# Kernel tuning notes

Hardware: AMD Instinct MI355X
Metric: run time of the kernel (lower is better)

Reference implementation:

```python
import jax, jax.numpy as jnp
import numpy as np

ANNEAL_T_START = 5.0
T_END = 1.0


def setup_inputs() -> dict:
    key = jax.random.key(0)
    ks = jax.random.split(key, 8)
    B, V, H, CD, WID = 8192, 1024, 128, 16, 64
    return {
        "cond": jax.random.normal(ks[0], (B, CD), jnp.float32),
        "W": 0.01 * jax.random.normal(ks[1], (V, H), jnp.float32),
        "b": 0.01 * jax.random.normal(ks[2], (V,), jnp.float32),
        "c": 0.01 * jax.random.normal(ks[3], (H,), jnp.float32),
        "fc1_w": jax.random.normal(ks[4], (WID, CD), jnp.float32) / np.float32(np.sqrt(CD)),
        "fc1_b": jnp.zeros((WID,), jnp.float32),
        "fc2_w": jax.random.normal(ks[5], (2 * (V + H), WID), jnp.float32) / np.float32(np.sqrt(WID)),
        "fc2_b": jnp.zeros((2 * (V + H),), jnp.float32),
        "falloff": jnp.float32(1.0),
        "steps": 16,
    }


def _bern(key, p):
    # Bernoulli sample as float of same dtype as p.
    return (jax.random.uniform(key, p.shape, p.dtype) < p).astype(p.dtype)


def reference(cond, W, b, c, fc1_w, fc1_b, fc2_w, fc2_b, falloff, steps):
    V, H = W.shape
    B = cond.shape[0]
    dtype = W.dtype

    # Conditioner: FiLM-style modulation of visible/hidden biases.
    x = jnp.tanh(cond @ fc1_w.T + fc1_b)
    x = x @ fc2_w.T + fc2_b  # [B, 2*(V+H)]
    gamma_b = x[:, :V]
    beta_b = x[:, V:2 * V]
    gamma_c = x[:, 2 * V:2 * V + H]
    beta_c = x[:, 2 * V + H:]
    b_mod = (1.0 + gamma_b) * b + beta_b  # [B, V]
    c_mod = (1.0 + gamma_c) * c + beta_c  # [B, H]
    bsum = jnp.sum(b_mod, axis=-1)  # [B], constant across steps

    # Annealing temperature schedule (sigmoid falloff).
    t = jnp.arange(steps, dtype=dtype)
    s = 1.0 / (1.0 + jnp.exp(falloff * (t - steps / 2.0)))
    temps = T_END + (ANNEAL_T_START - T_END) * s  # [steps]

    base = jax.random.key(42)
    v0 = _bern(jax.random.fold_in(base, 2 ** 20), jnp.full((B, V), 0.5, dtype))
    s0_0 = jnp.ones((B, 1), dtype)

    def flip(v, s0):
        return s0 * v + (1.0 - s0) * (1.0 - v)

    def step(carry, xs):
        v, s0 = carry
        i, T = xs
        k1, k2, k3 = jax.random.split(jax.random.fold_in(base, i), 3)
        v_eff = flip(v, s0)
        p_h = jax.nn.sigmoid((v_eff @ W + c_mod) / T)  # [B, H]
        h = _bern(k1, p_h)
        a = h @ W.T  # [B, V]
        vb = jnp.sum(v * b_mod, axis=-1)
        va = jnp.sum(v * a, axis=-1)
        dE = -bsum - jnp.sum(a, axis=-1) + 2.0 * vb + 2.0 * va  # [B]
        p_s0 = jax.nn.sigmoid(dE / T)
        s0n = _bern(k2, p_s0)[:, None]  # [B, 1]
        p_v = jax.nn.sigmoid((a + b_mod) / T)
        v_samp = _bern(k3, p_v)
        v_next = flip(v_samp, s0n)
        return (v_next, s0n), None

    (v, _), _ = jax.lax.scan(
        step, (v0, s0_0), (jnp.arange(steps, dtype=jnp.int32), temps)
    )
    return v
```

## Files before the change

### kernel.cpp

```cpp
#include <hip/hip_runtime.h>
#include <stdint.h>

#pragma clang fp contract(off)

#define B_ 8192
#define V_ 1024
#define H_ 128
#define CD_ 16
#define WID_ 64
#define NOUT_ 2304
#define STEPS_ 16

__host__ __device__ __forceinline__ void tf2x32(uint32_t k0, uint32_t k1,
                                                uint32_t x0, uint32_t x1,
                                                uint32_t* o0, uint32_t* o1) {
  uint32_t ks2 = k0 ^ k1 ^ 0x1BD11BDAu;
#define RL_(v, d) (((v) << (d)) | ((v) >> (32 - (d))))
#define RND_(a) { x0 += x1; x1 = RL_(x1, a); x1 ^= x0; }
  x0 += k0; x1 += k1;
  RND_(13) RND_(15) RND_(26) RND_(6)
  x0 += k1; x1 += ks2 + 1u;
  RND_(17) RND_(29) RND_(16) RND_(24)
  x0 += ks2; x1 += k0 + 2u;
  RND_(13) RND_(15) RND_(26) RND_(6)
  x0 += k0; x1 += k1 + 3u;
  RND_(17) RND_(29) RND_(16) RND_(24)
  x0 += k1; x1 += ks2 + 4u;
  RND_(13) RND_(15) RND_(26) RND_(6)
  x0 += ks2; x1 += k0 + 5u;
#undef RND_
#undef RL_
  *o0 = x0; *o1 = x1;
}

struct Keys { uint32_t a[6]; };

__device__ __forceinline__ uint32_t draw_bits(uint32_t ka, uint32_t kb, uint32_t j) {
  uint32_t x0, x1;
  tf2x32(ka, kb, 0u, j, &x0, &x1);
  return x0 ^ x1;
}

__device__ __forceinline__ float bits_to_u(uint32_t bits) {
  return __fsub_rn(__uint_as_float((bits >> 9) | 0x3f800000u), 1.0f);
}

__device__ __forceinline__ float exp_a(float x) {
  float xc = fminf(fmaxf(x, -88.3762626647949f), 88.3762626647950f);
  float fx = floorf(__fadd_rn(__fmul_rn(xc, 1.44269504088896341f), 0.5f));
  float xr = __fsub_rn(xc, __fmul_rn(0.693359375f, fx));
  xr = __fsub_rn(xr, __fmul_rn(-2.12194440e-4f, fx));
  float zz = __fmul_rn(xr, xr);
  float y = 1.9875691500E-4f;
  y = __fadd_rn(__fmul_rn(y, xr), 1.3981999507E-3f);
  y = __fadd_rn(__fmul_rn(y, xr), 8.3334519073E-3f);
  y = __fadd_rn(__fmul_rn(y, xr), 4.1665795894E-2f);
  y = __fadd_rn(__fmul_rn(y, xr), 1.6666665459E-1f);
  y = __fadd_rn(__fmul_rn(y, xr), 5.0000001201E-1f);
  y = __fadd_rn(__fmul_rn(y, zz), xr);
  y = __fadd_rn(y, 1.0f);
  int n = (int)fx;
  float sc = __int_as_float((n + 127) << 23);
  return __fmul_rn(y, sc);
}

__device__ __forceinline__ float tanh_a(float xin) {
  float x = fmaxf(fminf(xin, 7.90531110763549805f), -7.90531110763549805f);
  float x2 = __fmul_rn(x, x);
  float p = __fadd_rn(__fmul_rn(x2, -2.76076847742355e-16f), 2.00018790482477e-13f);
  p = __fadd_rn(__fmul_rn(x2, p), -8.60467152213735e-11f);
  p = __fadd_rn(__fmul_rn(x2, p), 5.12229709037114e-08f);
  p = __fadd_rn(__fmul_rn(x2, p), 1.48572235717979e-05f);
  p = __fadd_rn(__fmul_rn(x2, p), 6.37261928875436e-04f);
  p = __fadd_rn(__fmul_rn(x2, p), 4.89352455891786e-03f);
  p = __fmul_rn(x, p);
  float q = __fadd_rn(__fmul_rn(x2, 1.19825839466702e-06f), 1.18534705686654e-04f);
  q = __fadd_rn(__fmul_rn(x2, q), 2.26843463243900e-03f);
  q = __fadd_rn(__fmul_rn(x2, q), 4.89352518554385e-03f);
  float r = p / q;
  if (fabsf(xin) < 0.0004f) r = xin;
  return r;
}

__device__ __forceinline__ float sigmoid_a(float z) {
  float e = exp_a(-z);
  return 1.0f / __fadd_rn(1.0f, e);
}

__device__ __forceinline__ float maskf(float wv, uint32_t sm) {
  return __uint_as_float(__float_as_uint(wv) & sm);
}

__global__ void k_transpose(const float* __restrict__ W, float* __restrict__ WT,
                            const float* __restrict__ fc2w, float* __restrict__ fc2T) {
  int i = blockIdx.x * blockDim.x + threadIdx.x;
  if (i < V_ * H_) { int v = i / H_, h = i % H_; WT[h * V_ + v] = W[i]; }
  if (i < NOUT_ * WID_) { int j = i / WID_, w = i % WID_; fc2T[w * NOUT_ + j] = fc2w[i]; }
}

__global__ void k_temps(const float* __restrict__ falloff, float* __restrict__ temps) {
  int t = threadIdx.x;
  if (t < 16) {
    float arg = __fmul_rn(*falloff, __fsub_rn((float)t, 8.0f));
    float e = exp_a(arg);
    float s = 1.0f / __fadd_rn(1.0f, e);
    temps[t] = __fadd_rn(1.0f, __fmul_rn(4.0f, s));
  }
}

__global__ void k_mlp1(const float* __restrict__ cond, const float* __restrict__ fc1w,
                       const float* __restrict__ fc1b, float* __restrict__ xout) {
  int idx = blockIdx.x * blockDim.x + threadIdx.x;
  if (idx >= B_ * WID_) return;
  int row = idx >> 6, w = idx & 63;
  float acc = 0.0f;
  for (int k = 0; k < CD_; k++) acc = __fmaf_rn(cond[row * CD_ + k], fc1w[w * CD_ + k], acc);
  float z = __fadd_rn(acc, fc1b[w]);
  xout[idx] = tanh_a(z);
}

__global__ __launch_bounds__(128) void k_mlp2b(const float* __restrict__ xmlp,
                       const float* __restrict__ fc2T, const float* __restrict__ fc2b,
                       const float* __restrict__ bvec, float* __restrict__ b_mod) {
  __shared__ float xs[32][WID_];
  int jbase = blockIdx.x * 128;
  int r0 = blockIdx.y * 32;
  int tid = threadIdx.x;
  for (int t = tid; t < 32 * WID_; t += 128)
    xs[t >> 6][t & 63] = xmlp[(r0 + (t >> 6)) * WID_ + (t & 63)];
  __syncthreads();
  int j = jbase + tid;
  float accg[32], accb[32];
#pragma unroll
  for (int r = 0; r < 32; r++) { accg[r] = 0.0f; accb[r] = 0.0f; }
  for (int w = 0; w < WID_; w++) {
    float fg = fc2T[w * NOUT_ + j];
    float fb = fc2T[w * NOUT_ + 1024 + j];
#pragma unroll
    for (int r = 0; r < 32; r++) {
      float xv = xs[r][w];
      accg[r] = __fmaf_rn(xv, fg, accg[r]);
      accb[r] = __fmaf_rn(xv, fb, accb[r]);
    }
  }
  float bj = bvec[j];
  float biasg = fc2b[j], biasb = fc2b[1024 + j];
#pragma unroll
  for (int r = 0; r < 32; r++) {
    float g = __fadd_rn(accg[r], biasg);
    float bb = __fadd_rn(accb[r], biasb);
    float t1 = __fadd_rn(1.0f, g);
    b_mod[(r0 + r) * V_ + j] = __fadd_rn(__fmul_rn(t1, bj), bb);
  }
}

__global__ __launch_bounds__(128) void k_mlp2c(const float* __restrict__ xmlp,
                       const float* __restrict__ fc2T, const float* __restrict__ fc2b,
                       const float* __restrict__ cvec, float* __restrict__ c_mod) {
  __shared__ float xs[32][WID_];
  int r0 = blockIdx.y * 32;
  int tid = threadIdx.x;
  for (int t = tid; t < 32 * WID_; t += 128)
    xs[t >> 6][t & 63] = xmlp[(r0 + (t >> 6)) * WID_ + (t & 63)];
  __syncthreads();
  float accg[32], accb[32];
#pragma unroll
  for (int r = 0; r < 32; r++) { accg[r] = 0.0f; accb[r] = 0.0f; }
  for (int w = 0; w < WID_; w++) {
    float fg = fc2T[w * NOUT_ + 2048 + tid];
    float fb = fc2T[w * NOUT_ + 2176 + tid];
#pragma unroll
    for (int r = 0; r < 32; r++) {
      float xv = xs[r][w];
      accg[r] = __fmaf_rn(xv, fg, accg[r]);
      accb[r] = __fmaf_rn(xv, fb, accb[r]);
    }
  }
  float cj = cvec[tid];
  float biasg = fc2b[2048 + tid], biasb = fc2b[2176 + tid];
#pragma unroll
  for (int r = 0; r < 32; r++) {
    float g = __fadd_rn(accg[r], biasg);
    float bb = __fadd_rn(accb[r], biasb);
    float t1 = __fadd_rn(1.0f, g);
    c_mod[(r0 + r) * H_ + tid] = __fadd_rn(__fmul_rn(t1, cj), bb);
  }
}

__global__ __launch_bounds__(64) void k_bsum(const float* __restrict__ b_mod,
                                             float* __restrict__ bsum) {
  int row = blockIdx.x * 64 + threadIdx.x;
  const float4* bp = (const float4*)(b_mod + (size_t)row * V_);
  float acc = 0.0f;
  for (int c = 0; c < 32; c++) {
    float4 Bv[8];
#pragma unroll
    for (int q = 0; q < 8; q++) Bv[q] = bp[c * 8 + q];
#pragma unroll
    for (int q = 0; q < 8; q++) {
      acc = __fadd_rn(acc, Bv[q].x);
      acc = __fadd_rn(acc, Bv[q].y);
      acc = __fadd_rn(acc, Bv[q].z);
      acc = __fadd_rn(acc, Bv[q].w);
    }
  }
  bsum[row] = acc;
}

__global__ void k_v0(float* __restrict__ vout, uint32_t* __restrict__ v_bits,
                     float* __restrict__ s0, uint32_t kva, uint32_t kvb) {
  int idx = blockIdx.x * blockDim.x + threadIdx.x;
  int row = idx >> 10, col = idx & 1023;
  uint32_t bits = draw_bits(kva, kvb, (uint32_t)idx);
  float u = bits_to_u(bits);
  float v = (u < 0.5f) ? 1.0f : 0.0f;
  vout[idx] = v;
  unsigned long long m = __ballot(v == 1.0f);
  if ((threadIdx.x & 63) == 0) {
    v_bits[row * 32 + (col >> 5)] = (uint32_t)m;
    v_bits[row * 32 + (col >> 5) + 1] = (uint32_t)(m >> 32);
  }
  if (col == 0) s0[row] = 1.0f;
}

__global__ __launch_bounds__(256) void k_h(const float* __restrict__ W,
                   const float* __restrict__ c_mod, const uint32_t* __restrict__ v_bits,
                   const float* __restrict__ s0, uint32_t* __restrict__ h_bits,
                   const float* __restrict__ temps, int step, Keys kn) {
  __shared__ uint32_t nib[16][32];
  int tid = threadIdx.x;
  int ct = tid & 31;
  int rt = tid >> 5;
  int h0 = ct << 2;
  int row0 = blockIdx.x * 16 + rt * 2;
  float T = temps[step];
  float acc0[4] = {0.f, 0.f, 0.f, 0.f};
  float acc1[4] = {0.f, 0.f, 0.f, 0.f};
  uint32_t flip0 = (s0[row0] == 0.0f) ? 0xFFFFFFFFu : 0u;
  uint32_t flip1 = (s0[row0 + 1] == 0.0f) ? 0xFFFFFFFFu : 0u;
  const uint4* vb0 = (const uint4*)(v_bits + (size_t)row0 * 32);
  const uint4* vb1 = (const uint4*)(v_bits + (size_t)(row0 + 1) * 32);
  const float* wbase = W + h0;

  auto sect = [&](uint32_t w0, uint32_t w1, const float* wp) {
    uint32_t m0 = __brev(w0) ^ flip0;
    uint32_t m1 = __brev(w1) ^ flip1;
    for (int j4 = 0; j4 < 8; j4++) {
#pragma unroll
      for (int jj = 0; jj < 4; jj++) {
        float4 wv = *(const float4*)(wp + (size_t)jj * H_);
        uint32_t s0m = (uint32_t)((int32_t)m0 >> 31);
        uint32_t s1m = (uint32_t)((int32_t)m1 >> 31);
        m0 <<= 1; m1 <<= 1;
        acc0[0] = __fadd_rn(acc0[0], maskf(wv.x, s0m));
        acc0[1] = __fadd_rn(acc0[1], maskf(wv.y, s0m));
        acc0[2] = __fadd_rn(acc0[2], maskf(wv.z, s0m));
        acc0[3] = __fadd_rn(acc0[3], maskf(wv.w, s0m));
        acc1[0] = __fadd_rn(acc1[0], maskf(wv.x, s1m));
        acc1[1] = __fadd_rn(acc1[1], maskf(wv.y, s1m));
        acc1[2] = __fadd_rn(acc1[2], maskf(wv.z, s1m));
        acc1[3] = __fadd_rn(acc1[3], maskf(wv.w, s1m));
      }
      wp += (size_t)4 * H_;
    }
  };

  for (int kq = 0; kq < 8; kq++) {
    uint4 q0 = vb0[kq];
    uint4 q1 = vb1[kq];
    const float* wk = wbase + (size_t)(kq * 128) * H_;
    sect(q0.x, q1.x, wk);
    sect(q0.y, q1.y, wk + (size_t)32 * H_);
    sect(q0.z, q1.z, wk + (size_t)64 * H_);
    sect(q0.w, q1.w, wk + (size_t)96 * H_);
  }

  uint32_t nib0 = 0, nib1 = 0;
  float4 cm0 = *(const float4*)(c_mod + (size_t)row0 * H_ + h0);
  float4 cm1 = *(const float4*)(c_mod + (size_t)(row0 + 1) * H_ + h0);
  const float cm0a[4] = {cm0.x, cm0.y, cm0.z, cm0.w};
  const float cm1a[4] = {cm1.x, cm1.y, cm1.z, cm1.w};
#pragma unroll
  for (int e = 0; e < 4; e++) {
    float z0 = __fadd_rn(acc0[e], cm0a[e]) / T;
    float p0 = sigmoid_a(z0);
    uint32_t b0 = draw_bits(kn.a[0], kn.a[1], (uint32_t)(row0 * H_ + h0 + e));
    if (bits_to_u(b0) < p0) nib0 |= 1u << e;
    float z1 = __fadd_rn(acc1[e], cm1a[e]) / T;
    float p1 = sigmoid_a(z1);
    uint32_t b1 = draw_bits(kn.a[0], kn.a[1], (uint32_t)((row0 + 1) * H_ + h0 + e));
    if (bits_to_u(b1) < p1) nib1 |= 1u << e;
  }
  nib[rt * 2][ct] = nib0;
  nib[rt * 2 + 1][ct] = nib1;
  __syncthreads();
  if (tid < 64) {
    int rloc = tid >> 2, wq = tid & 3;
    uint32_t word = 0;
#pragma unroll
    for (int i = 0; i < 8; i++) word |= nib[rloc][wq * 8 + i] << (4 * i);
    h_bits[(size_t)(blockIdx.x * 16 + rloc) * 4 + wq] = word;
  }
}

__global__ __launch_bounds__(256) void k_a(const float* __restrict__ WT,
                   const uint32_t* __restrict__ h_bits, float* __restrict__ a) {
  int tid = threadIdx.x;
  int ct = tid & 63;
  int rt = __builtin_amdgcn_readfirstlane(tid >> 6);
  int v0 = blockIdx.x * 256 + (ct << 2);
  int r0 = blockIdx.y * 32 + rt * 8;
  float acc[8][4];
#pragma unroll
  for (int r = 0; r < 8; r++)
#pragma unroll
    for (int e = 0; e < 4; e++) acc[r][e] = 0.0f;
  uint4 hw[8];
#pragma unroll
  for (int r = 0; r < 8; r++) hw[r] = *(const uint4*)(h_bits + (size_t)(r0 + r) * 4);
  const float* wp0 = WT + v0;

  auto asect = [&](int WW, const uint32_t mwin[8]) {
    uint32_t m[8];
#pragma unroll
    for (int r = 0; r < 8; r++) m[r] = __brev(mwin[r]);
    const float* wp = wp0 + (size_t)(WW * 32) * V_;
    for (int j4 = 0; j4 < 8; j4++) {
#pragma unroll
      for (int jj = 0; jj < 4; jj++) {
        float4 wv = *(const float4*)(wp + (size_t)jj * V_);
#pragma unroll
        for (int r = 0; r < 8; r++) {
          uint32_t sm = (uint32_t)((int32_t)m[r] >> 31);
          m[r] <<= 1;
          acc[r][0] = __fadd_rn(acc[r][0], maskf(wv.x, sm));
          acc[r][1] = __fadd_rn(acc[r][1], maskf(wv.y, sm));
          acc[r][2] = __fadd_rn(acc[r][2], maskf(wv.z, sm));
          acc[r][3] = __fadd_rn(acc[r][3], maskf(wv.w, sm));
        }
      }
      wp += (size_t)4 * V_;
    }
  };

  {
    uint32_t mw[8];
#pragma unroll
    for (int r = 0; r < 8; r++) mw[r] = hw[r].x;
    asect(0, mw);
#pragma unroll
    for (int r = 0; r < 8; r++) mw[r] = hw[r].y;
    asect(1, mw);
#pragma unroll
    for (int r = 0; r < 8; r++) mw[r] = hw[r].z;
    asect(2, mw);
#pragma unroll
    for (int r = 0; r < 8; r++) mw[r] = hw[r].w;
    asect(3, mw);
  }

#pragma unroll
  for (int r = 0; r < 8; r++) {
    float4 o = make_float4(acc[r][0], acc[r][1], acc[r][2], acc[r][3]);
    *(float4*)(a + (size_t)(r0 + r) * V_ + v0) = o;
  }
}

__global__ __launch_bounds__(64) void k_s0(const float* __restrict__ a,
                     const float* __restrict__ b_mod, const float* __restrict__ bsum,
                     const uint32_t* __restrict__ v_bits, float* __restrict__ s0,
                     const float* __restrict__ temps, int step, Keys kn) {
  int row = blockIdx.x * 64 + threadIdx.x;
  const float4* ap = (const float4*)(a + (size_t)row * V_);
  const float4* bp = (const float4*)(b_mod + (size_t)row * V_);
  const uint32_t* vbp = v_bits + row * 32;
  float suma = 0.0f, vb = 0.0f, va = 0.0f;
  float4 A0[8], B0[8], A1[8], B1[8];
  uint32_t m0, m1;

  auto LOADC = [&](int c, float4* A, float4* B, uint32_t& m) {
#pragma unroll
    for (int q = 0; q < 8; q++) { A[q] = ap[c * 8 + q]; B[q] = bp[c * 8 + q]; }
    m = vbp[c];
  };
  auto PROC = [&](const float4* A, const float4* B, uint32_t m) {
#pragma unroll
    for (int q = 0; q < 8; q++) {
      const float ax[4] = {A[q].x, A[q].y, A[q].z, A[q].w};
      const float bx[4] = {B[q].x, B[q].y, B[q].z, B[q].w};
#pragma unroll
      for (int e = 0; e < 4; e++) {
        float bit = (float)((m >> (q * 4 + e)) & 1u);
        suma = __fadd_rn(suma, ax[e]);
        vb = __fmaf_rn(bx[e], bit, vb);
        va = __fmaf_rn(ax[e], bit, va);
      }
    }
  };

  LOADC(0, A0, B0, m0);
  for (int cc = 0; cc < 16; cc++) {
    LOADC(2 * cc + 1, A1, B1, m1);
    PROC(A0, B0, m0);
    if (cc < 15) LOADC(2 * cc + 2, A0, B0, m0);
    PROC(A1, B1, m1);
  }

  float dE = __fsub_rn(-bsum[row], suma);
  dE = __fadd_rn(dE, __fmul_rn(2.0f, vb));
  dE = __fadd_rn(dE, __fmul_rn(2.0f, va));
  float T = temps[step];
  float p = sigmoid_a(dE / T);
  uint32_t bits = draw_bits(kn.a[2], kn.a[3], (uint32_t)row);
  float u = bits_to_u(bits);
  s0[row] = (u < p) ? 1.0f : 0.0f;
}

__global__ void k_v(const float* __restrict__ a, const float* __restrict__ b_mod,
                    const float* __restrict__ s0, float* __restrict__ vout,
                    uint32_t* __restrict__ v_bits, const float* __restrict__ temps, int step,
                    Keys kn) {
  int idx = blockIdx.x * blockDim.x + threadIdx.x;
  int row = idx >> 10, col = idx & 1023;
  float T = temps[step];
  float z = __fadd_rn(a[idx], b_mod[idx]) / T;
  float p = sigmoid_a(z);
  uint32_t bits = draw_bits(kn.a[4], kn.a[5], (uint32_t)idx);
  float u = bits_to_u(bits);
  float vs = (u < p) ? 1.0f : 0.0f;
  float vn = (s0[row] != 0.0f) ? vs : (1.0f - vs);
  vout[idx] = vn;
  unsigned long long m = __ballot(vn == 1.0f);
  if ((threadIdx.x & 63) == 0) {
    v_bits[row * 32 + (col >> 5)] = (uint32_t)m;
    v_bits[row * 32 + (col >> 5) + 1] = (uint32_t)(m >> 32);
  }
}

extern "C" void kernel_launch(void* const* d_in, const int* in_sizes, int n_in,
                              void* d_out, int out_size, void* d_ws, size_t ws_size,
                              hipStream_t stream) {
  const float* cond = (const float*)d_in[0];
  const float* W = (const float*)d_in[1];
  const float* bvec = (const float*)d_in[2];
  const float* cvec = (const float*)d_in[3];
  const float* fc1w = (const float*)d_in[4];
  const float* fc1b = (const float*)d_in[5];
  const float* fc2w = (const float*)d_in[6];
  const float* fc2b = (const float*)d_in[7];
  const float* falloff = (const float*)d_in[8];
  float* out = (float*)d_out;

  char* ws = (char*)d_ws;
  size_t off = 0;
  auto alloc = [&](size_t bytes) { void* p = ws + off; off += (bytes + 255) & ~(size_t)255; return p; };
  float* b_mod = (float*)alloc((size_t)B_ * V_ * 4);
  float* c_mod = (float*)alloc((size_t)B_ * H_ * 4);
  float* abuf  = (float*)alloc((size_t)B_ * V_ * 4);
  float* xmlp  = (float*)alloc((size_t)B_ * WID_ * 4);
  float* bsum  = (float*)alloc((size_t)B_ * 4);
  float* s0    = (float*)alloc((size_t)B_ * 4);
  uint32_t* v_bits = (uint32_t*)alloc((size_t)B_ * 32 * 4);
  uint32_t* h_bits = (uint32_t*)alloc((size_t)B_ * 4 * 4);
  float* WT    = (float*)alloc((size_t)H_ * V_ * 4);
  float* fc2T  = (float*)alloc((size_t)WID_ * NOUT_ * 4);
  float* temps = (float*)alloc(16 * 4);

  uint32_t kva, kvb;
  tf2x32(0u, 42u, 0u, 1048576u, &kva, &kvb);
  Keys kn[16];
  for (int i = 0; i < 16; i++) {
    uint32_t f0, f1;
    tf2x32(0u, 42u, 0u, (uint32_t)i, &f0, &f1);
    uint32_t a0, a1;
    tf2x32(f0, f1, 0u, 0u, &a0, &a1); kn[i].a[0] = a0; kn[i].a[1] = a1;
    tf2x32(f0, f1, 0u, 1u, &a0, &a1); kn[i].a[2] = a0; kn[i].a[3] = a1;
    tf2x32(f0, f1, 0u, 2u, &a0, &a1); kn[i].a[4] = a0; kn[i].a[5] = a1;
  }

  k_transpose<<<(NOUT_ * WID_ + 255) / 256, 256, 0, stream>>>(W, WT, fc2w, fc2T);
  k_temps<<<1, 64, 0, stream>>>(falloff, temps);
  k_mlp1<<<(B_ * WID_) / 256, 256, 0, stream>>>(cond, fc1w, fc1b, xmlp);
  k_mlp2b<<<dim3(8, 256), 128, 0, stream>>>(xmlp, fc2T, fc2b, bvec, b_mod);
  k_mlp2c<<<dim3(1, 256), 128, 0, stream>>>(xmlp, fc2T, fc2b, cvec, c_mod);
  k_bsum<<<B_ / 64, 64, 0, stream>>>(b_mod, bsum);
  k_v0<<<(B_ * V_) / 256, 256, 0, stream>>>(out, v_bits, s0, kva, kvb);

  for (int i = 0; i < STEPS_; i++) {
    k_h<<<B_ / 16, 256, 0, stream>>>(W, c_mod, v_bits, s0, h_bits, temps, i, kn[i]);
    k_a<<<dim3(4, B_ / 32), 256, 0, stream>>>(WT, h_bits, abuf);
    k_s0<<<B_ / 64, 64, 0, stream>>>(abuf, b_mod, bsum, v_bits, s0, temps, i, kn[i]);
    k_v<<<(B_ * V_) / 256, 256, 0, stream>>>(abuf, b_mod, s0, out, v_bits, temps, i, kn[i]);
  }
}
```

Baseline: 3.498 ms.

## Use packed FP32 FMA with 0/1 multipliers and give k_h four rows per thread

The masked-add accumulation in k_h and k_a now multiplies each weight by a 0.0 or 1.0 factor taken from the bit mask and uses v_pk_fma_f32, which handles two lanes per instruction. The aim is to halve the VALU instruction count of the inner loops. k_h also moves to 128-thread blocks with four rows per thread, so each weight load is reused across more rows. Adding w*0 instead of a masked zero keeps results the same for finite weights, though the register use of the wider per-thread tile could lower occupancy.

```diff
diff --git a/kernel.cpp b/kernel.cpp
--- a/kernel.cpp
+++ b/kernel.cpp
@@ -10,6 +10,12 @@
 #define WID_ 64
 #define NOUT_ 2304
 #define STEPS_ 16
+
+typedef float f32x2 __attribute__((ext_vector_type(2)));
+
+__device__ __forceinline__ void pkfma(f32x2& acc, f32x2 wv, f32x2 bf2) {
+  asm("v_pk_fma_f32 %0, %1, %2, %0" : "+v"(acc) : "v"(wv), "v"(bf2));
+}
 
 __host__ __device__ __forceinline__ void tf2x32(uint32_t k0, uint32_t k1,
                                                 uint32_t x0, uint32_t x1,
@@ -87,10 +93,6 @@
   return 1.0f / __fadd_rn(1.0f, e);
 }
 
-__device__ __forceinline__ float maskf(float wv, uint32_t sm) {
-  return __uint_as_float(__float_as_uint(wv) & sm);
-}
-
 __global__ void k_transpose(const float* __restrict__ W, float* __restrict__ WT,
                             const float* __restrict__ fc2w, float* __restrict__ fc2T) {
   int i = blockIdx.x * blockDim.x + threadIdx.x;
@@ -223,7 +225,7 @@
   if (col == 0) s0[row] = 1.0f;
 }
 
-__global__ __launch_bounds__(256) void k_h(const float* __restrict__ W,
+__global__ __launch_bounds__(128) void k_h(const float* __restrict__ W,
                    const float* __restrict__ c_mod, const uint32_t* __restrict__ v_bits,
                    const float* __restrict__ s0, uint32_t* __restrict__ h_bits,
                    const float* __restrict__ temps, int step, Keys kn) {
@@ -232,67 +234,74 @@
   int ct = tid & 31;
   int rt = tid >> 5;
   int h0 = ct << 2;
-  int row0 = blockIdx.x * 16 + rt * 2;
+  int row0 = blockIdx.x * 16 + rt * 4;
   float T = temps[step];
-  float acc0[4] = {0.f, 0.f, 0.f, 0.f};
-  float acc1[4] = {0.f, 0.f, 0.f, 0.f};
-  uint32_t flip0 = (s0[row0] == 0.0f) ? 0xFFFFFFFFu : 0u;
-  uint32_t flip1 = (s0[row0 + 1] == 0.0f) ? 0xFFFFFFFFu : 0u;
+  f32x2 acc[4][2];
+#pragma unroll
+  for (int r = 0; r < 4; r++) { acc[r][0] = f32x2{0.f, 0.f}; acc[r][1] = f32x2{0.f, 0.f}; }
+  uint32_t flip[4];
+#pragma unroll
+  for (int r = 0; r < 4; r++) flip[r] = (s0[row0 + r] == 0.0f) ? 0xFFFFFFFFu : 0u;
+  const float* wbase = W + h0;
+
+  auto sect = [&](uint32_t w0, uint32_t w1, uint32_t w2, uint32_t w3, const float* wp) {
+    uint32_t m[4];
+    m[0] = __brev(w0) ^ flip[0];
+    m[1] = __brev(w1) ^ flip[1];
+    m[2] = __brev(w2) ^ flip[2];
+    m[3] = __brev(w3) ^ flip[3];
+    for (int j4 = 0; j4 < 8; j4++) {
+#pragma unroll
+      for (int jj = 0; jj < 4; jj++) {
+        float4 wv = *(const float4*)(wp + (size_t)jj * H_);
+        f32x2 wlo = {wv.x, wv.y};
+        f32x2 whi = {wv.z, wv.w};
+#pragma unroll
+        for (int r = 0; r < 4; r++) {
+          uint32_t sm = (uint32_t)((int32_t)m[r] >> 31);
+          m[r] <<= 1;
+          float bf = __uint_as_float(sm & 0x3f800000u);
+          f32x2 b2 = {bf, bf};
+          pkfma(acc[r][0], wlo, b2);
+          pkfma(acc[r][1], whi, b2);
+        }
+      }
+      wp += (size_t)4 * H_;
+    }
+  };
+
   const uint4* vb0 = (const uint4*)(v_bits + (size_t)row0 * 32);
   const uint4* vb1 = (const uint4*)(v_bits + (size_t)(row0 + 1) * 32);
-  const float* wbase = W + h0;
-
-  auto sect = [&](uint32_t w0, uint32_t w1, const float* wp) {
-    uint32_t m0 = __brev(w0) ^ flip0;
-    uint32_t m1 = __brev(w1) ^ flip1;
-    for (int j4 = 0; j4 < 8; j4++) {
-#pragma unroll
-      for (int jj = 0; jj < 4; jj++) {
-        float4 wv = *(const float4*)(wp + (size_t)jj * H_);
-        uint32_t s0m = (uint32_t)((int32_t)m0 >> 31);
-        uint32_t s1m = (uint32_t)((int32_t)m1 >> 31);
-        m0 <<= 1; m1 <<= 1;
-        acc0[0] = __fadd_rn(acc0[0], maskf(wv.x, s0m));
-        acc0[1] = __fadd_rn(acc0[1], maskf(wv.y, s0m));
-        acc0[2] = __fadd_rn(acc0[2], maskf(wv.z, s0m));
-        acc0[3] = __fadd_rn(acc0[3], maskf(wv.w, s0m));
-        acc1[0] = __fadd_rn(acc1[0], maskf(wv.x, s1m));
-        acc1[1] = __fadd_rn(acc1[1], maskf(wv.y, s1m));
-        acc1[2] = __fadd_rn(acc1[2], maskf(wv.z, s1m));
-        acc1[3] = __fadd_rn(acc1[3], maskf(wv.w, s1m));
-      }
-      wp += (size_t)4 * H_;
-    }
-  };
-
+  const uint4* vb2 = (const uint4*)(v_bits + (size_t)(row0 + 2) * 32);
+  const uint4* vb3 = (const uint4*)(v_bits + (size_t)(row0 + 3) * 32);
   for (int kq = 0; kq < 8; kq++) {
     uint4 q0 = vb0[kq];
     uint4 q1 = vb1[kq];
+    uint4 q2 = vb2[kq];
+    uint4 q3 = vb3[kq];
     const float* wk = wbase + (size_t)(kq * 128) * H_;
-    sect(q0.x, q1.x, wk);
-    sect(q0.y, q1.y, wk + (size_t)32 * H_);
-    sect(q0.z, q1.z, wk + (size_t)64 * H_);
-    sect(q0.w, q1.w, wk + (size_t)96 * H_);
-  }
-
-  uint32_t nib0 = 0, nib1 = 0;
-  float4 cm0 = *(const float4*)(c_mod + (size_t)row0 * H_ + h0);
-  float4 cm1 = *(const float4*)(c_mod + (size_t)(row0 + 1) * H_ + h0);
-  const float cm0a[4] = {cm0.x, cm0.y, cm0.z, cm0.w};
-  const float cm1a[4] = {cm1.x, cm1.y, cm1.z, cm1.w};
-#pragma unroll
-  for (int e = 0; e < 4; e++) {
-    float z0 = __fadd_rn(acc0[e], cm0a[e]) / T;
-    float p0 = sigmoid_a(z0);
-    uint32_t b0 = draw_bits(kn.a[0], kn.a[1], (uint32_t)(row0 * H_ + h0 + e));
-    if (bits_to_u(b0) < p0) nib0 |= 1u << e;
-    float z1 = __fadd_rn(acc1[e], cm1a[e]) / T;
-    float p1 = sigmoid_a(z1);
-    uint32_t b1 = draw_bits(kn.a[0], kn.a[1], (uint32_t)((row0 + 1) * H_ + h0 + e));
-    if (bits_to_u(b1) < p1) nib1 |= 1u << e;
-  }
-  nib[rt * 2][ct] = nib0;
-  nib[rt * 2 + 1][ct] = nib1;
+    sect(q0.x, q1.x, q2.x, q3.x, wk);
+    sect(q0.y, q1.y, q2.y, q3.y, wk + (size_t)32 * H_);
+    sect(q0.z, q1.z, q2.z, q3.z, wk + (size_t)64 * H_);
+    sect(q0.w, q1.w, q2.w, q3.w, wk + (size_t)96 * H_);
+  }
+
+#pragma unroll
+  for (int r = 0; r < 4; r++) {
+    int row = row0 + r;
+    float4 cm = *(const float4*)(c_mod + (size_t)row * H_ + h0);
+    const float cma[4] = {cm.x, cm.y, cm.z, cm.w};
+    const float ac[4] = {acc[r][0][0], acc[r][0][1], acc[r][1][0], acc[r][1][1]};
+    uint32_t nb = 0;
+#pragma unroll
+    for (int e = 0; e < 4; e++) {
+      float z = __fadd_rn(ac[e], cma[e]) / T;
+      float p = sigmoid_a(z);
+      uint32_t b = draw_bits(kn.a[0], kn.a[1], (uint32_t)(row * H_ + h0 + e));
+      if (bits_to_u(b) < p) nb |= 1u << e;
+    }
+    nib[rt * 4 + r][ct] = nb;
+  }
   __syncthreads();
   if (tid < 64) {
     int rloc = tid >> 2, wq = tid & 3;
@@ -307,14 +316,12 @@
                    const uint32_t* __restrict__ h_bits, float* __restrict__ a) {
   int tid = threadIdx.x;
   int ct = tid & 63;
-  int rt = __builtin_amdgcn_readfirstlane(tid >> 6);
+  int rt = tid >> 6;
   int v0 = blockIdx.x * 256 + (ct << 2);
   int r0 = blockIdx.y * 32 + rt * 8;
-  float acc[8][4];
-#pragma unroll
-  for (int r = 0; r < 8; r++)
-#pragma unroll
-    for (int e = 0; e < 4; e++) acc[r][e] = 0.0f;
+  f32x2 acc[8][2];
+#pragma unroll
+  for (int r = 0; r < 8; r++) { acc[r][0] = f32x2{0.f, 0.f}; acc[r][1] = f32x2{0.f, 0.f}; }
   uint4 hw[8];
 #pragma unroll
   for (int r = 0; r < 8; r++) hw[r] = *(const uint4*)(h_bits + (size_t)(r0 + r) * 4);
@@ -329,14 +336,16 @@
 #pragma unroll
       for (int jj = 0; jj < 4; jj++) {
         float4 wv = *(const float4*)(wp + (size_t)jj * V_);
+        f32x2 wlo = {wv.x, wv.y};
+        f32x2 whi = {wv.z, wv.w};
 #pragma unroll
         for (int r = 0; r < 8; r++) {
           uint32_t sm = (uint32_t)((int32_t)m[r] >> 31);
           m[r] <<= 1;
-          acc[r][0] = __fadd_rn(acc[r][0], maskf(wv.x, sm));
-          acc[r][1] = __fadd_rn(acc[r][1], maskf(wv.y, sm));
-          acc[r][2] = __fadd_rn(acc[r][2], maskf(wv.z, sm));
-          acc[r][3] = __fadd_rn(acc[r][3], maskf(wv.w, sm));
+          float bf = __uint_as_float(sm & 0x3f800000u);
+          f32x2 b2 = {bf, bf};
+          pkfma(acc[r][0], wlo, b2);
+          pkfma(acc[r][1], whi, b2);
         }
       }
       wp += (size_t)4 * V_;
@@ -361,7 +370,7 @@
 
 #pragma unroll
   for (int r = 0; r < 8; r++) {
-    float4 o = make_float4(acc[r][0], acc[r][1], acc[r][2], acc[r][3]);
+    float4 o = make_float4(acc[r][0][0], acc[r][0][1], acc[r][1][0], acc[r][1][1]);
     *(float4*)(a + (size_t)(r0 + r) * V_ + v0) = o;
   }
 }
@@ -487,7 +496,7 @@
   k_v0<<<(B_ * V_) / 256, 256, 0, stream>>>(out, v_bits, s0, kva, kvb);
 
   for (int i = 0; i < STEPS_; i++) {
-    k_h<<<B_ / 16, 256, 0, stream>>>(W, c_mod, v_bits, s0, h_bits, temps, i, kn[i]);
+    k_h<<<B_ / 16, 128, 0, stream>>>(W, c_mod, v_bits, s0, h_bits, temps, i, kn[i]);
     k_a<<<dim3(4, B_ / 32), 256, 0, stream>>>(WT, h_bits, abuf);
     k_s0<<<B_ / 64, 64, 0, stream>>>(abuf, b_mod, bsum, v_bits, s0, temps, i, kn[i]);
     k_v<<<(B_ * V_) / 256, 256, 0, stream>>>(abuf, b_mod, s0, out, v_bits, temps, i, kn[i]);
```

Measured after the change: 3.580 ms. +2.3%, slower.
